# Kernel optimization log

Measured on AMD Instinct MI355X. Metric: run time of the kernel, lower is better.

The kernel has to match this reference:

```python
import jax, jax.numpy as jnp
import numpy as np

S = 7  # output_size
B, C, HF, WF = 8, 256, 160, 160
N = 128
IMG = 640


def setup_inputs() -> dict:
    key = jax.random.key(0)
    k1, k2, k3, k4 = jax.random.split(key, 4)
    feature_map = jax.random.normal(k1, (B, C, HF, WF), jnp.float32)
    # boxes in image-pixel coordinates (the module divides by image_size itself)
    pts = jax.random.uniform(k2, (B, N, 2, 2), jnp.float32, 0.0, float(IMG))
    lo = jnp.min(pts, axis=2)  # (x1, y1)
    hi = jnp.max(pts, axis=2)  # (x2, y2)
    bboxes = jnp.concatenate([lo, hi], axis=-1)  # [B, N, 4]
    proj_w = jax.random.normal(k3, (C, C), jnp.float32) * (1.0 / np.sqrt(C))
    proj_b = jax.random.normal(k4, (C,), jnp.float32) * 0.01
    return {"feature_map": feature_map, "bboxes": bboxes,
            "proj_w": proj_w, "proj_b": proj_b,
            "image_h": IMG, "image_w": IMG}


def _forward(feature_map, bboxes, proj_w, proj_b, image_h, image_w):
    Bb, Cc, Hf, Wf = feature_map.shape
    # 1x1 conv projection
    f = jnp.einsum('bchw,oc->bohw', feature_map, proj_w) + proj_b[None, :, None, None]
    # scale boxes from image coords to feature coords, then integer clip (as in torch code)
    sx = float(Wf) / float(image_w)
    sy = float(Hf) / float(image_h)
    x1 = jnp.clip(jnp.floor(bboxes[..., 0] * sx).astype(jnp.int32), 0, Wf - 1)
    y1 = jnp.clip(jnp.floor(bboxes[..., 1] * sy).astype(jnp.int32), 0, Hf - 1)
    x2 = jnp.clip(jnp.floor(bboxes[..., 2] * sx).astype(jnp.int32), x1 + 1, Wf)
    y2 = jnp.clip(jnp.floor(bboxes[..., 3] * sy).astype(jnp.int32), y1 + 1, Hf)
    Lx = x2 - x1  # [B, N], >= 1 by construction
    Ly = y2 - y1
    i = jnp.arange(S, dtype=jnp.int32)
    # adaptive_avg_pool2d bin edges: start=floor(i*L/S), end=ceil((i+1)*L/S)
    rs = y1[..., None] + (i * Ly[..., None]) // S            # [B, N, S]
    re = y1[..., None] + ((i + 1) * Ly[..., None] + S - 1) // S
    cs = x1[..., None] + (i * Lx[..., None]) // S
    ce = x1[..., None] + ((i + 1) * Lx[..., None] + S - 1) // S
    # summed-area table (zero-padded): I[b,c,y,x] = sum of f[b,c,:y,:x]
    I = jnp.cumsum(jnp.cumsum(f, axis=2), axis=3)
    I = jnp.pad(I, ((0, 0), (0, 0), (1, 0), (1, 0)))

    def per_batch(Ib, rs_b, re_b, cs_b, ce_b):
        # Ib: [C, Hf+1, Wf+1]; index arrays: [N, S]
        tl = Ib[:, rs_b[:, :, None], cs_b[:, None, :]]
        tr = Ib[:, rs_b[:, :, None], ce_b[:, None, :]]
        bl = Ib[:, re_b[:, :, None], cs_b[:, None, :]]
        br = Ib[:, re_b[:, :, None], ce_b[:, None, :]]
        return br - tr - bl + tl  # [C, N, S, S]

    sums = jax.vmap(per_batch)(I, rs, re, cs, ce)  # [B, C, N, S, S]
    counts = ((re - rs)[..., :, None] * (ce - cs)[..., None, :]).astype(f.dtype)  # [B, N, S, S]
    region_features = jnp.transpose(sums, (0, 2, 1, 3, 4)) / counts[:, :, None, :, :]
    # area in raw bbox units, as in the original code
    area_ratios = (bboxes[..., 2] - bboxes[..., 0]) * (bboxes[..., 3] - bboxes[..., 1])
    return region_features, area_ratios


def reference(feature_map, bboxes, proj_w, proj_b, image_h, image_w):
    return _forward(feature_map, bboxes, proj_w, proj_b, image_h, image_w)
```

## Files before the change

### kernel.cpp

```cpp
#include <hip/hip_runtime.h>
#include <hip/hip_bf16.h>

#define BB 8
#define NN 128
#define CC 256
#define HFD 160
#define WFD 160
#define SS 7
#define REGION_OUT_ELEMS (8*128*256*49)

typedef short short8 __attribute__((ext_vector_type(8)));
typedef float f32x4  __attribute__((ext_vector_type(4)));

__global__ __launch_bounds__(256) void k0_convert_w(const float* __restrict__ W,
                                                    __hip_bfloat16* __restrict__ Wb) {
    int o = blockIdx.x;
    int c = threadIdx.x;
    Wb[o * CC + c] = __float2bfloat16(W[o * CC + c]);
}

__global__ __launch_bounds__(256) void k1_rowsum_transpose(const float* __restrict__ fm,
                                                           float* __restrict__ R) {
    int bid = blockIdx.x;
    int cq  = bid & 3;
    int bh  = bid >> 2;
    int h   = bh % HFD;
    int b   = bh / HFD;
    int c0  = cq * 64;
    int t   = threadIdx.x;

    __shared__ float tile[64][161];
    __shared__ float segsum[64][5];

    #pragma unroll
    for (int it = 0; it < 10; ++it) {
        int vid = it * 256 + t;
        int c_l = vid / 40;
        int wq  = vid - c_l * 40;
        f32x4 v = __builtin_nontemporal_load(
            (const f32x4*)(fm + (((size_t)(b * CC + c0 + c_l)) * HFD + h) * WFD + wq * 4));
        tile[c_l][wq * 4 + 0] = v.x;
        tile[c_l][wq * 4 + 1] = v.y;
        tile[c_l][wq * 4 + 2] = v.z;
        tile[c_l][wq * 4 + 3] = v.w;
    }
    __syncthreads();

    int seg = t >> 6;
    int row = t & 63;
    {
        float s = 0.f;
        int w0 = seg * 40;
        #pragma unroll 8
        for (int k = 0; k < 40; ++k) {
            s += tile[row][w0 + k];
            tile[row][w0 + k] = s;
        }
        segsum[row][seg] = s;
    }
    __syncthreads();
    if (t < 64) {
        float a0 = segsum[t][0];
        float a1 = a0 + segsum[t][1];
        float a2 = a1 + segsum[t][2];
        segsum[t][1] = a0;
        segsum[t][2] = a1;
        segsum[t][3] = a2;
    }
    __syncthreads();
    if (seg > 0) {
        float off = segsum[row][seg];
        int w0 = seg * 40;
        #pragma unroll 8
        for (int k = 0; k < 40; ++k) tile[row][w0 + k] += off;
    }
    __syncthreads();

    size_t obase = (((size_t)b * HFD + h) * WFD) * CC + c0;
    #pragma unroll
    for (int it = 0; it < 10; ++it) {
        int vid = it * 256 + t;
        int w   = vid >> 4;
        int cg  = vid & 15;
        float4 o;
        o.x = tile[cg * 4 + 0][w];
        o.y = tile[cg * 4 + 1][w];
        o.z = tile[cg * 4 + 2][w];
        o.w = tile[cg * 4 + 3][w];
        *(float4*)(R + obase + (size_t)w * CC + cg * 4) = o;
    }
}

__global__ __launch_bounds__(256) void k2_colsum(float* __restrict__ I) {
    int w = blockIdx.x % WFD;
    int b = blockIdx.x / WFD;
    int c = threadIdx.x;
    float* p = I + (((size_t)b * HFD) * WFD + w) * CC + c;
    const size_t stride = (size_t)WFD * CC;
    float s = 0.f;
    #pragma unroll 16
    for (int h = 0; h < HFD; ++h) {
        float v = p[(size_t)h * stride];
        s += v;
        p[(size_t)h * stride] = s;
    }
}

#define PB_STRIDE 264

__global__ __launch_bounds__(256) void k3_gather_gemm(
        const float* __restrict__ I, const __hip_bfloat16* __restrict__ Wb,
        const float* __restrict__ bias, const float* __restrict__ bboxes,
        const int* __restrict__ ih_p, const int* __restrict__ iw_p,
        float* __restrict__ out) {
    int bn = blockIdx.x;
    int b  = bn >> 7;
    int t  = threadIdx.x;

    __shared__ __hip_bfloat16 Pb[64 * PB_STRIDE];

    float bx1 = bboxes[bn * 4 + 0];
    float by1 = bboxes[bn * 4 + 1];
    float bx2 = bboxes[bn * 4 + 2];
    float by2 = bboxes[bn * 4 + 3];
    float sx = (float)WFD / (float)iw_p[0];
    float sy = (float)HFD / (float)ih_p[0];

    int x1 = min(max((int)floorf(bx1 * sx), 0), WFD - 1);
    int y1 = min(max((int)floorf(by1 * sy), 0), HFD - 1);
    int x2 = min(max((int)floorf(bx2 * sx), x1 + 1), WFD);
    int y2 = min(max((int)floorf(by2 * sy), y1 + 1), HFD);
    int Lx = x2 - x1, Ly = y2 - y1;

    int rs[SS], re[SS], cs[SS], ce[SS];
    #pragma unroll
    for (int i = 0; i < SS; ++i) {
        rs[i] = y1 + (i * Ly) / SS;
        re[i] = y1 + ((i + 1) * Ly + SS - 1) / SS;
        cs[i] = x1 + (i * Lx) / SS;
        ce[i] = x1 + ((i + 1) * Lx + SS - 1) / SS;
    }

    #pragma unroll
    for (int r = 49; r < 64; ++r) Pb[r * PB_STRIDE + t] = __float2bfloat16(0.f);

    {
        const int c = t;
        const size_t Ib = (size_t)b * HFD * WFD * CC;
        #pragma unroll
        for (int i = 0; i < SS; ++i) {
            int r0 = rs[i] - 1, r1 = re[i] - 1;
            float rh = (float)(re[i] - rs[i]);
            #pragma unroll
            for (int j = 0; j < SS; ++j) {
                int c0 = cs[j] - 1, c1 = ce[j] - 1;
                float br = I[Ib + ((size_t)(r1 * WFD + c1)) * CC + c];
                float tr = (r0 >= 0) ? I[Ib + ((size_t)(r0 * WFD + c1)) * CC + c] : 0.f;
                float bl = (c0 >= 0) ? I[Ib + ((size_t)(r1 * WFD + c0)) * CC + c] : 0.f;
                float tl = (r0 >= 0 && c0 >= 0) ? I[Ib + ((size_t)(r0 * WFD + c0)) * CC + c] : 0.f;
                float cnt = rh * (float)(ce[j] - cs[j]);
                Pb[(i * SS + j) * PB_STRIDE + c] = __float2bfloat16((br - tr - bl + tl) / cnt);
            }
        }
    }
    __syncthreads();

    {
        const int lane = t & 63;
        const int wv   = t >> 6;
        const int ln   = lane & 15;
        const int quad = lane >> 4;
        const int ob0  = wv * 64;

        f32x4 z = {0.f, 0.f, 0.f, 0.f};
        f32x4 acc[4][4];
        #pragma unroll
        for (int mt = 0; mt < 4; ++mt)
            #pragma unroll
            for (int nt = 0; nt < 4; ++nt) acc[mt][nt] = z;

        #pragma unroll
        for (int k0 = 0; k0 < CC; k0 += 32) {
            short8 a[4], bf[4];
            #pragma unroll
            for (int mt = 0; mt < 4; ++mt)
                a[mt] = *(const short8*)((const short*)Wb + (ob0 + mt * 16 + ln) * CC + k0 + quad * 8);
            #pragma unroll
            for (int nt = 0; nt < 4; ++nt)
                bf[nt] = *(const short8*)((const short*)Pb + (nt * 16 + ln) * PB_STRIDE + k0 + quad * 8);
            #pragma unroll
            for (int mt = 0; mt < 4; ++mt)
                #pragma unroll
                for (int nt = 0; nt < 4; ++nt)
                    acc[mt][nt] = __builtin_amdgcn_mfma_f32_16x16x32_bf16(a[mt], bf[nt], acc[mt][nt], 0, 0, 0);
        }

        size_t obase = (size_t)bn * CC * 49;
        #pragma unroll
        for (int mt = 0; mt < 4; ++mt) {
            f32x4 bv = *(const f32x4*)(bias + ob0 + mt * 16 + quad * 4);
            #pragma unroll
            for (int nt = 0; nt < 4; ++nt) {
                int cell = nt * 16 + ln;
                if (cell < 49) {
                    #pragma unroll
                    for (int reg = 0; reg < 4; ++reg) {
                        int o = ob0 + mt * 16 + quad * 4 + reg;
                        __builtin_nontemporal_store(acc[mt][nt][reg] + bv[reg],
                                                    &out[obase + (size_t)o * 49 + cell]);
                    }
                }
            }
        }
    }

    if (t == 0) {
        __builtin_nontemporal_store((bx2 - bx1) * (by2 - by1), &out[REGION_OUT_ELEMS + bn]);
    }
}

extern "C" void kernel_launch(void* const* d_in, const int* in_sizes, int n_in,
                              void* d_out, int out_size, void* d_ws, size_t ws_size,
                              hipStream_t stream) {
    const float* fm     = (const float*)d_in[0];
    const float* bboxes = (const float*)d_in[1];
    const float* W      = (const float*)d_in[2];
    const float* bias   = (const float*)d_in[3];
    const int*   ih     = (const int*)d_in[4];
    const int*   iw     = (const int*)d_in[5];
    float* out = (float*)d_out;

    __hip_bfloat16* Wb = (__hip_bfloat16*)d_ws;
    float* I = (float*)((char*)d_ws + (size_t)CC * CC * 2 + 256);
    I = (float*)(((uintptr_t)I + 1023) & ~(uintptr_t)1023);

    k0_convert_w<<<CC, 256, 0, stream>>>(W, Wb);
    k1_rowsum_transpose<<<BB * HFD * 4, 256, 0, stream>>>(fm, I);
    k2_colsum<<<BB * WFD, 256, 0, stream>>>(I);
    k3_gather_gemm<<<BB * NN, 256, 0, stream>>>(I, Wb, bias, bboxes, ih, iw, out);
}
```

Measured before the change: 450.2 us.

## Split fused gather+GEMM kernel into separate gather and GEMM kernels

The fused per-box kernel is split in two. A 512-thread gather kernel splits the 49 cells across two halves of the block and writes bf16 pooled features to a global workspace. A separate GEMM kernel then reads them, along with the weights, for the MFMA projection. The aim is more parallelism and latency hiding in the gather phase, and a GEMM kernel free of gather register pressure. The cost is an extra launch and a global round trip for the pooled matrix.

```diff
diff --git a/kernel.cpp b/kernel.cpp
--- a/kernel.cpp
+++ b/kernel.cpp
@@ -106,18 +106,15 @@
     }
 }
 
-#define PB_STRIDE 264
-
-__global__ __launch_bounds__(256) void k3_gather_gemm(
-        const float* __restrict__ I, const __hip_bfloat16* __restrict__ Wb,
-        const float* __restrict__ bias, const float* __restrict__ bboxes,
+__global__ __launch_bounds__(512) void k3a_gather(
+        const float* __restrict__ I, const float* __restrict__ bboxes,
         const int* __restrict__ ih_p, const int* __restrict__ iw_p,
-        float* __restrict__ out) {
+        __hip_bfloat16* __restrict__ Pm, float* __restrict__ out) {
     int bn = blockIdx.x;
     int b  = bn >> 7;
     int t  = threadIdx.x;
-
-    __shared__ __hip_bfloat16 Pb[64 * PB_STRIDE];
+    int c  = t & 255;
+    int half = t >> 8;
 
     float bx1 = bboxes[bn * 4 + 0];
     float by1 = bboxes[bn * 4 + 1];
@@ -141,81 +138,92 @@
         ce[i] = x1 + ((i + 1) * Lx + SS - 1) / SS;
     }
 
-    #pragma unroll
-    for (int r = 49; r < 64; ++r) Pb[r * PB_STRIDE + t] = __float2bfloat16(0.f);
-
-    {
-        const int c = t;
-        const size_t Ib = (size_t)b * HFD * WFD * CC;
-        #pragma unroll
-        for (int i = 0; i < SS; ++i) {
-            int r0 = rs[i] - 1, r1 = re[i] - 1;
-            float rh = (float)(re[i] - rs[i]);
-            #pragma unroll
-            for (int j = 0; j < SS; ++j) {
-                int c0 = cs[j] - 1, c1 = ce[j] - 1;
-                float br = I[Ib + ((size_t)(r1 * WFD + c1)) * CC + c];
-                float tr = (r0 >= 0) ? I[Ib + ((size_t)(r0 * WFD + c1)) * CC + c] : 0.f;
-                float bl = (c0 >= 0) ? I[Ib + ((size_t)(r1 * WFD + c0)) * CC + c] : 0.f;
-                float tl = (r0 >= 0 && c0 >= 0) ? I[Ib + ((size_t)(r0 * WFD + c0)) * CC + c] : 0.f;
-                float cnt = rh * (float)(ce[j] - cs[j]);
-                Pb[(i * SS + j) * PB_STRIDE + c] = __float2bfloat16((br - tr - bl + tl) / cnt);
-            }
-        }
-    }
-    __syncthreads();
-
-    {
-        const int lane = t & 63;
-        const int wv   = t >> 6;
-        const int ln   = lane & 15;
-        const int quad = lane >> 4;
-        const int ob0  = wv * 64;
-
-        f32x4 z = {0.f, 0.f, 0.f, 0.f};
-        f32x4 acc[4][4];
+    const size_t Ib = (size_t)b * HFD * WFD * CC;
+    __hip_bfloat16* pmb = Pm + (size_t)bn * 64 * CC;
+
+#define GATHER_CELL(cell)                                                        \
+    {                                                                            \
+        const int i_ = (cell) / SS, j_ = (cell) % SS;                            \
+        int r0 = rs[i_] - 1, r1 = re[i_] - 1;                                    \
+        int c0 = cs[j_] - 1, c1 = ce[j_] - 1;                                    \
+        float br = I[Ib + ((size_t)(r1 * WFD + c1)) * CC + c];                   \
+        float tr = (r0 >= 0) ? I[Ib + ((size_t)(r0 * WFD + c1)) * CC + c] : 0.f; \
+        float bl = (c0 >= 0) ? I[Ib + ((size_t)(r1 * WFD + c0)) * CC + c] : 0.f; \
+        float tl = (r0 >= 0 && c0 >= 0) ? I[Ib + ((size_t)(r0 * WFD + c0)) * CC + c] : 0.f; \
+        float cnt = (float)(re[i_] - rs[i_]) * (float)(ce[j_] - cs[j_]);         \
+        pmb[(cell) * CC + c] = __float2bfloat16((br - tr - bl + tl) / cnt);      \
+    }
+
+    if (half == 0) {
+        #pragma unroll
+        for (int k = 0; k < 25; ++k) GATHER_CELL(k);
+    } else {
+        #pragma unroll
+        for (int k = 25; k < 49; ++k) GATHER_CELL(k);
+        __hip_bfloat16 z = __float2bfloat16(0.f);
+        #pragma unroll
+        for (int r = 49; r < 64; ++r) pmb[r * CC + c] = z;
+    }
+#undef GATHER_CELL
+
+    if (t == 0) {
+        __builtin_nontemporal_store((bx2 - bx1) * (by2 - by1), &out[REGION_OUT_ELEMS + bn]);
+    }
+}
+
+__global__ __launch_bounds__(256) void k3b_gemm(
+        const __hip_bfloat16* __restrict__ Wb, const __hip_bfloat16* __restrict__ Pm,
+        const float* __restrict__ bias, float* __restrict__ out) {
+    int bn = blockIdx.x;
+    int t  = threadIdx.x;
+    const int lane = t & 63;
+    const int wv   = t >> 6;
+    const int ln   = lane & 15;
+    const int quad = lane >> 4;
+    const int ob0  = wv * 64;
+
+    const short* A  = (const short*)Wb;
+    const short* Bm = (const short*)(Pm + (size_t)bn * 64 * CC);
+
+    f32x4 z = {0.f, 0.f, 0.f, 0.f};
+    f32x4 acc[4][4];
+    #pragma unroll
+    for (int mt = 0; mt < 4; ++mt)
+        #pragma unroll
+        for (int nt = 0; nt < 4; ++nt) acc[mt][nt] = z;
+
+    #pragma unroll
+    for (int k0 = 0; k0 < CC; k0 += 32) {
+        short8 a[4], bf[4];
+        #pragma unroll
+        for (int mt = 0; mt < 4; ++mt)
+            a[mt] = *(const short8*)(A + (ob0 + mt * 16 + ln) * CC + k0 + quad * 8);
+        #pragma unroll
+        for (int nt = 0; nt < 4; ++nt)
+            bf[nt] = *(const short8*)(Bm + (nt * 16 + ln) * CC + k0 + quad * 8);
         #pragma unroll
         for (int mt = 0; mt < 4; ++mt)
             #pragma unroll
-            for (int nt = 0; nt < 4; ++nt) acc[mt][nt] = z;
-
-        #pragma unroll
-        for (int k0 = 0; k0 < CC; k0 += 32) {
-            short8 a[4], bf[4];
-            #pragma unroll
-            for (int mt = 0; mt < 4; ++mt)
-                a[mt] = *(const short8*)((const short*)Wb + (ob0 + mt * 16 + ln) * CC + k0 + quad * 8);
-            #pragma unroll
             for (int nt = 0; nt < 4; ++nt)
-                bf[nt] = *(const short8*)((const short*)Pb + (nt * 16 + ln) * PB_STRIDE + k0 + quad * 8);
-            #pragma unroll
-            for (int mt = 0; mt < 4; ++mt)
+                acc[mt][nt] = __builtin_amdgcn_mfma_f32_16x16x32_bf16(a[mt], bf[nt], acc[mt][nt], 0, 0, 0);
+    }
+
+    size_t obase = (size_t)bn * CC * 49;
+    #pragma unroll
+    for (int mt = 0; mt < 4; ++mt) {
+        f32x4 bv = *(const f32x4*)(bias + ob0 + mt * 16 + quad * 4);
+        #pragma unroll
+        for (int nt = 0; nt < 4; ++nt) {
+            int cell = nt * 16 + ln;
+            if (cell < 49) {
                 #pragma unroll
-                for (int nt = 0; nt < 4; ++nt)
-                    acc[mt][nt] = __builtin_amdgcn_mfma_f32_16x16x32_bf16(a[mt], bf[nt], acc[mt][nt], 0, 0, 0);
-        }
-
-        size_t obase = (size_t)bn * CC * 49;
-        #pragma unroll
-        for (int mt = 0; mt < 4; ++mt) {
-            f32x4 bv = *(const f32x4*)(bias + ob0 + mt * 16 + quad * 4);
-            #pragma unroll
-            for (int nt = 0; nt < 4; ++nt) {
-                int cell = nt * 16 + ln;
-                if (cell < 49) {
-                    #pragma unroll
-                    for (int reg = 0; reg < 4; ++reg) {
-                        int o = ob0 + mt * 16 + quad * 4 + reg;
-                        __builtin_nontemporal_store(acc[mt][nt][reg] + bv[reg],
-                                                    &out[obase + (size_t)o * 49 + cell]);
-                    }
+                for (int reg = 0; reg < 4; ++reg) {
+                    int o = ob0 + mt * 16 + quad * 4 + reg;
+                    __builtin_nontemporal_store(acc[mt][nt][reg] + bv[reg],
+                                                &out[obase + (size_t)o * 49 + cell]);
                 }
             }
         }
-    }
-
-    if (t == 0) {
-        __builtin_nontemporal_store((bx2 - bx1) * (by2 - by1), &out[REGION_OUT_ELEMS + bn]);
     }
 }
 
@@ -233,9 +241,12 @@
     __hip_bfloat16* Wb = (__hip_bfloat16*)d_ws;
     float* I = (float*)((char*)d_ws + (size_t)CC * CC * 2 + 256);
     I = (float*)(((uintptr_t)I + 1023) & ~(uintptr_t)1023);
+    __hip_bfloat16* Pm = (__hip_bfloat16*)((char*)I + (size_t)BB * HFD * WFD * CC * 4);
+    Pm = (__hip_bfloat16*)(((uintptr_t)Pm + 1023) & ~(uintptr_t)1023);
 
     k0_convert_w<<<CC, 256, 0, stream>>>(W, Wb);
     k1_rowsum_transpose<<<BB * HFD * 4, 256, 0, stream>>>(fm, I);
     k2_colsum<<<BB * WFD, 256, 0, stream>>>(I);
-    k3_gather_gemm<<<BB * NN, 256, 0, stream>>>(I, Wb, bias, bboxes, ih, iw, out);
-}
+    k3a_gather<<<BB * NN, 512, 0, stream>>>(I, bboxes, ih, iw, Pm, out);
+    k3b_gemm<<<BB * NN, 256, 0, stream>>>(Wb, Pm, bias, out);
+}
```

After: 461.5 us. +2.5%, slower.

## Vectorize SAT gather per channel-quad and split gather-GEMM across 8 waves

Applied to the files above, without the earlier changes.

The gather/GEMM kernel now runs with 512 threads. Each wave owns a set of pooling cells, and each lane loads four channels at once with float4 reads of the summed-area table. The corner masking is done arithmetically instead of with branches, and a reciprocal replaces the per-element division. The MFMA projection is split so each of the 8 waves computes 32 output channels instead of 64, which lowers per-thread accumulator pressure and adds wave parallelism. The explicit zero fill of the padded Pb rows is removed; those rows only feed output columns that are never stored.

```diff
diff --git a/kernel.cpp b/kernel.cpp
--- a/kernel.cpp
+++ b/kernel.cpp
@@ -108,7 +108,7 @@
 
 #define PB_STRIDE 264
 
-__global__ __launch_bounds__(256) void k3_gather_gemm(
+__global__ __launch_bounds__(512) void k3_gather_gemm(
         const float* __restrict__ I, const __hip_bfloat16* __restrict__ Wb,
         const float* __restrict__ bias, const float* __restrict__ bboxes,
         const int* __restrict__ ih_p, const int* __restrict__ iw_p,
@@ -116,6 +116,8 @@
     int bn = blockIdx.x;
     int b  = bn >> 7;
     int t  = threadIdx.x;
+    const int lane = t & 63;
+    const int wv   = t >> 6;
 
     __shared__ __hip_bfloat16 Pb[64 * PB_STRIDE];
 
@@ -132,64 +134,76 @@
     int y2 = min(max((int)floorf(by2 * sy), y1 + 1), HFD);
     int Lx = x2 - x1, Ly = y2 - y1;
 
-    int rs[SS], re[SS], cs[SS], ce[SS];
-    #pragma unroll
-    for (int i = 0; i < SS; ++i) {
-        rs[i] = y1 + (i * Ly) / SS;
-        re[i] = y1 + ((i + 1) * Ly + SS - 1) / SS;
-        cs[i] = x1 + (i * Lx) / SS;
-        ce[i] = x1 + ((i + 1) * Lx + SS - 1) / SS;
-    }
-
-    #pragma unroll
-    for (int r = 49; r < 64; ++r) Pb[r * PB_STRIDE + t] = __float2bfloat16(0.f);
-
     {
-        const int c = t;
-        const size_t Ib = (size_t)b * HFD * WFD * CC;
-        #pragma unroll
-        for (int i = 0; i < SS; ++i) {
-            int r0 = rs[i] - 1, r1 = re[i] - 1;
-            float rh = (float)(re[i] - rs[i]);
-            #pragma unroll
-            for (int j = 0; j < SS; ++j) {
-                int c0 = cs[j] - 1, c1 = ce[j] - 1;
-                float br = I[Ib + ((size_t)(r1 * WFD + c1)) * CC + c];
-                float tr = (r0 >= 0) ? I[Ib + ((size_t)(r0 * WFD + c1)) * CC + c] : 0.f;
-                float bl = (c0 >= 0) ? I[Ib + ((size_t)(r1 * WFD + c0)) * CC + c] : 0.f;
-                float tl = (r0 >= 0 && c0 >= 0) ? I[Ib + ((size_t)(r0 * WFD + c0)) * CC + c] : 0.f;
-                float cnt = rh * (float)(ce[j] - cs[j]);
-                Pb[(i * SS + j) * PB_STRIDE + c] = __float2bfloat16((br - tr - bl + tl) / cnt);
+        const float* Ibl = I + (size_t)b * HFD * WFD * CC + 4 * lane;
+        unsigned short* pbs = (unsigned short*)Pb;
+
+        #pragma unroll
+        for (int k = 0; k < 7; ++k) {
+            int cell = wv + 8 * k;
+            int cc_  = min(cell, 48);
+            int i_ = cc_ / SS, j_ = cc_ % SS;
+
+            int rs_ = y1 + (i_ * Ly) / SS;
+            int re_ = y1 + ((i_ + 1) * Ly + SS - 1) / SS;
+            int cs_ = x1 + (j_ * Lx) / SS;
+            int ce_ = x1 + ((j_ + 1) * Lx + SS - 1) / SS;
+
+            int r1 = re_ - 1;
+            int r0 = max(rs_ - 1, 0);
+            int c1 = ce_ - 1;
+            int c0 = max(cs_ - 1, 0);
+            float rm = (rs_ > 0) ? 1.f : 0.f;
+            float cm = (cs_ > 0) ? 1.f : 0.f;
+
+            f32x4 br = *(const f32x4*)(Ibl + ((size_t)(r1 * WFD + c1)) * CC);
+            f32x4 tr = *(const f32x4*)(Ibl + ((size_t)(r0 * WFD + c1)) * CC);
+            f32x4 bl = *(const f32x4*)(Ibl + ((size_t)(r1 * WFD + c0)) * CC);
+            f32x4 tl = *(const f32x4*)(Ibl + ((size_t)(r0 * WFD + c0)) * CC);
+
+            f32x4 s = (br - tr * rm) - (bl - tl * rm) * cm;
+            float inv = 1.f / ((float)(re_ - rs_) * (float)(ce_ - cs_));
+
+            ushort4 pk;
+            {
+                __hip_bfloat16 h0 = __float2bfloat16(s.x * inv);
+                __hip_bfloat16 h1 = __float2bfloat16(s.y * inv);
+                __hip_bfloat16 h2 = __float2bfloat16(s.z * inv);
+                __hip_bfloat16 h3 = __float2bfloat16(s.w * inv);
+                pk.x = *(unsigned short*)&h0;
+                pk.y = *(unsigned short*)&h1;
+                pk.z = *(unsigned short*)&h2;
+                pk.w = *(unsigned short*)&h3;
             }
+            *(ushort4*)(pbs + cell * PB_STRIDE + 4 * lane) = pk;
         }
     }
     __syncthreads();
 
     {
-        const int lane = t & 63;
-        const int wv   = t >> 6;
         const int ln   = lane & 15;
         const int quad = lane >> 4;
-        const int ob0  = wv * 64;
+        const int ob0  = wv * 32;
 
         f32x4 z = {0.f, 0.f, 0.f, 0.f};
-        f32x4 acc[4][4];
-        #pragma unroll
-        for (int mt = 0; mt < 4; ++mt)
+        f32x4 acc[2][4];
+        #pragma unroll
+        for (int mt = 0; mt < 2; ++mt)
             #pragma unroll
             for (int nt = 0; nt < 4; ++nt) acc[mt][nt] = z;
 
+        const short* A = (const short*)Wb;
         #pragma unroll
         for (int k0 = 0; k0 < CC; k0 += 32) {
-            short8 a[4], bf[4];
-            #pragma unroll
-            for (int mt = 0; mt < 4; ++mt)
-                a[mt] = *(const short8*)((const short*)Wb + (ob0 + mt * 16 + ln) * CC + k0 + quad * 8);
+            short8 a[2], bf[4];
+            #pragma unroll
+            for (int mt = 0; mt < 2; ++mt)
+                a[mt] = *(const short8*)(A + (ob0 + mt * 16 + ln) * CC + k0 + quad * 8);
             #pragma unroll
             for (int nt = 0; nt < 4; ++nt)
                 bf[nt] = *(const short8*)((const short*)Pb + (nt * 16 + ln) * PB_STRIDE + k0 + quad * 8);
             #pragma unroll
-            for (int mt = 0; mt < 4; ++mt)
+            for (int mt = 0; mt < 2; ++mt)
                 #pragma unroll
                 for (int nt = 0; nt < 4; ++nt)
                     acc[mt][nt] = __builtin_amdgcn_mfma_f32_16x16x32_bf16(a[mt], bf[nt], acc[mt][nt], 0, 0, 0);
@@ -197,7 +211,7 @@
 
         size_t obase = (size_t)bn * CC * 49;
         #pragma unroll
-        for (int mt = 0; mt < 4; ++mt) {
+        for (int mt = 0; mt < 2; ++mt) {
             f32x4 bv = *(const f32x4*)(bias + ob0 + mt * 16 + quad * 4);
             #pragma unroll
             for (int nt = 0; nt < 4; ++nt) {
@@ -237,5 +251,5 @@
     k0_convert_w<<<CC, 256, 0, stream>>>(W, Wb);
     k1_rowsum_transpose<<<BB * HFD * 4, 256, 0, stream>>>(fm, I);
     k2_colsum<<<BB * WFD, 256, 0, stream>>>(I);
-    k3_gather_gemm<<<BB * NN, 256, 0, stream>>>(I, Wb, bias, bboxes, ih, iw, out);
-}
+    k3_gather_gemm<<<BB * NN, 512, 0, stream>>>(I, Wb, bias, bboxes, ih, iw, out);
+}
```

Result: faster. 427.5 us (-5.0%).
